# Performance work log

Measured on AMD Instinct MI355X. Metric: run time of the kernel, lower is better.

The kernel has to match this reference:

```python
import jax, jax.numpy as jnp
import numpy as np

BN_EPS = 1e-5
N_SH, N_SS, N_HH, D = 1195, 390, 805, 64


def _gcn(x, edge_index, W, b, n_nodes, mean):
    # per-edge message = Linear(x_j); lin(x)[src] == lin(x[src])
    h = x @ W + b                                   # [N, out]
    msg = h[edge_index[0]]                          # gather sources -> [E, out]
    agg = jax.ops.segment_sum(msg, edge_index[1], num_segments=n_nodes)
    if mean:
        cnt = jax.ops.segment_sum(jnp.ones((edge_index.shape[1],), x.dtype),
                                  edge_index[1], num_segments=n_nodes)
        agg = agg / jnp.maximum(cnt, 1.0)[:, None]
    return jnp.tanh(agg)


def _bn(x, gamma, beta):
    # BatchNorm1d in training mode: biased batch statistics
    m = jnp.mean(x, axis=0)
    v = jnp.var(x, axis=0)
    return (x - m) * jax.lax.rsqrt(v + BN_EPS) * gamma + beta


def setup_inputs() -> dict:
    key = jax.random.key(0)
    ks = jax.random.split(key, 40)
    f32 = jnp.float32

    def lin(k, din, dout):
        k1, k2 = jax.random.split(k)
        s = 1.0 / np.sqrt(din)
        W = jax.random.uniform(k1, (din, dout), f32, -s, s)
        b = jax.random.uniform(k2, (dout,), f32, -s, s)
        return W, b

    inp = {}
    inp["x_SH"] = jnp.arange(N_SH, dtype=jnp.int64 if jax.config.jax_enable_x64 else jnp.int32)
    inp["edge_index_SH"] = jax.random.randint(ks[0], (2, 1_000_000), 0, N_SH)
    inp["x_SS"] = jnp.arange(N_SS)
    inp["edge_index_SS"] = jax.random.randint(ks[1], (2, 200_000), 0, N_SS)
    inp["x_HH"] = jnp.arange(N_HH)
    inp["edge_index_HH"] = jax.random.randint(ks[2], (2, 200_000), 0, N_HH)
    inp["prescription"] = jax.random.uniform(ks[3], (20000, N_SS), f32)
    inp["kgOneHot"] = jax.random.uniform(ks[4], (N_HH, 27), f32)

    inp["emb"] = jax.random.normal(ks[5], (N_SH, D), f32)
    inp["w_sh1"], inp["b_sh1"] = lin(ks[6], D, D)
    inp["w_sh2"], inp["b_sh2"] = lin(ks[7], D, D)
    inp["w_mlp1"], inp["b_mlp1"] = lin(ks[8], D, 256)
    inp["g_bn1"] = jnp.ones((256,), f32); inp["be_bn1"] = jnp.zeros((256,), f32)
    inp["w_sh1h"], inp["b_sh1h"] = lin(ks[9], D, D)
    inp["w_sh2h"], inp["b_sh2h"] = lin(ks[10], D, D)
    inp["w_mlp1h"], inp["b_mlp1h"] = lin(ks[11], D, 256)
    inp["g_bn1h"] = jnp.ones((256,), f32); inp["be_bn1h"] = jnp.zeros((256,), f32)
    inp["w_ss"], inp["b_ss"] = lin(ks[12], D, 256)
    inp["w_hh"], inp["b_hh"] = lin(ks[13], D + 27, 256)
    inp["w_mlp"], inp["b_mlp"] = lin(ks[14], 256, 256)
    inp["g_si"] = jnp.ones((256,), f32); inp["be_si"] = jnp.zeros((256,), f32)
    return inp


def reference(x_SH, edge_index_SH, x_SS, edge_index_SS, x_HH, edge_index_HH,
              prescription, kgOneHot, emb,
              w_sh1, b_sh1, w_sh2, b_sh2, w_mlp1, b_mlp1, g_bn1, be_bn1,
              w_sh1h, b_sh1h, w_sh2h, b_sh2h, w_mlp1h, b_mlp1h, g_bn1h, be_bn1h,
              w_ss, b_ss, w_hh, b_hh, w_mlp, b_mlp, g_si, be_si):
    # symptom branch on SH graph (mean aggregation)
    x1 = emb[x_SH]                                           # [1195, 64]
    x2 = _gcn(x1, edge_index_SH, w_sh1, b_sh1, N_SH, mean=True)
    x6 = _gcn(x2, edge_index_SH, w_sh2, b_sh2, N_SH, mean=True)
    x9 = (x1 + x2 + x6) / 3.0
    x9 = jnp.tanh(_bn(x9 @ w_mlp1 + b_mlp1, g_bn1, be_bn1))  # [1195, 256]

    # herb branch on SH graph
    x22 = _gcn(x1, edge_index_SH, w_sh1h, b_sh1h, N_SH, mean=True)
    x66 = _gcn(x22, edge_index_SH, w_sh2h, b_sh2h, N_SH, mean=True)
    x99 = (x1 + x22 + x66) / 3.0
    x99 = jnp.tanh(_bn(x99 @ w_mlp1h + b_mlp1h, g_bn1h, be_bn1h))

    # SS graph (add aggregation)
    x_ss1 = _gcn(emb[x_SS], edge_index_SS, w_ss, b_ss, N_SS, mean=False)  # [390, 256]

    # HH graph with KG one-hot features appended
    x_hh0 = jnp.concatenate([emb[x_HH], kgOneHot], axis=-1)  # [805, 91]
    x_hh1 = _gcn(x_hh0, edge_index_HH, w_hh, b_hh, N_HH, mean=False)      # [805, 256]

    es = x9[:N_SS] + x_ss1                                   # [390, 256]
    eh = x99[N_SS:] + x_hh1                                  # [805, 256]

    e_synd = prescription @ es                               # [B, 256]
    pre_sum = jnp.sum(prescription, axis=1, keepdims=True)
    e = e_synd / pre_sum
    e = jax.nn.relu(_bn(e @ w_mlp + b_mlp, g_si, be_si))
    return e @ eh.T                                          # [B, 805]
```

## Files before the change

### kernel.cpp

```cpp
#include <hip/hip_runtime.h>
#include <cstddef>
#include <cstdint>

#define N_SH 1195
#define N_SS 390
#define N_HH 805
#define DIM  64

typedef __bf16 bf16_t;
typedef bf16_t bf16x4v __attribute__((ext_vector_type(4)));
typedef bf16_t bf16x8v __attribute__((ext_vector_type(8)));
typedef float f32x4 __attribute__((ext_vector_type(4)));

__device__ inline ushort f2bf(float f) {
    union { float f; uint32_t u; } c; c.f = f;
    uint32_t u = c.u;
    u += 0x7FFFu + ((u >> 16) & 1u);
    return (ushort)(u >> 16);
}

__device__ inline void xcd_swizzle(int gx, int gy, int& bx, int& by) {
    int nwg = gx * gy;
    int lin = by * gx + bx;
    int q = nwg >> 3, r = nwg & 7;
    int xcd = lin & 7, idx = lin >> 3;
    int nt = (xcd < r ? xcd * (q + 1) : r * (q + 1) + (xcd - r) * q) + idx;
    by = nt / gx; bx = nt % gx;
}

__global__ void build_adj3_kernel(
    const int* __restrict__ e1, int E1, int hs1, uint32_t* __restrict__ T1,
    const int* __restrict__ e2, int E2, int hs2, uint32_t* __restrict__ T2,
    const int* __restrict__ e3, int E3, int hs3, uint32_t* __restrict__ T3)
{
    int i = blockIdx.x * blockDim.x + threadIdx.x;
    if (i < E1) {
        int src = e1[i], dst = e1[E1 + i];
        atomicAdd(&T1[(size_t)dst * hs1 + (src >> 2)], 1u << ((src & 3) * 8));
    } else if (i < E1 + E2) {
        int j = i - E1;
        int src = e2[j], dst = e2[E2 + j];
        atomicAdd(&T2[(size_t)dst * hs2 + (src >> 2)], 1u << ((src & 3) * 8));
    } else if (i < E1 + E2 + E3) {
        int j = i - E1 - E2;
        int src = e3[j], dst = e3[E3 + j];
        atomicAdd(&T3[(size_t)dst * hs3 + (src >> 2)], 1u << ((src & 3) * 8));
    }
}

__global__ void rowsum_inv_packed_kernel(const uint32_t* __restrict__ T, int R,
                                         int halfStride, float* __restrict__ inv) {
    int row  = blockIdx.x * (blockDim.x / 64) + (threadIdx.x / 64);
    int lane = threadIdx.x & 63;
    if (row >= R) return;
    const uint32_t* p = T + (size_t)row * halfStride;
    uint32_t s = 0;
    for (int c = lane; c < halfStride; c += 64) {
        uint32_t w = p[c];
        s += (w & 0xFFu) + ((w >> 8) & 0xFFu) + ((w >> 16) & 0xFFu) + (w >> 24);
    }
    for (int off = 32; off > 0; off >>= 1) s += __shfl_down(s, off);
    if (lane == 0) inv[row] = 1.0f / fmaxf((float)s, 1.0f);
}

__device__ inline void unpack_one(const uint32_t* __restrict__ T, int R, int C,
                                  int hs, ushort* __restrict__ out, int Cp, int i) {
    int r = i / Cp, c = i % Cp;
    float v = 0.f;
    if (r < R && c < C) {
        uint32_t w = T[(size_t)r * hs + (c >> 2)];
        v = (float)((w >> ((c & 3) * 8)) & 0xFFu);
    }
    out[i] = f2bf(v);
}

__global__ void cvt_unpack3_kernel(
    const uint32_t* __restrict__ T1, int hs1, ushort* __restrict__ o1, int n1, int Cp1,
    const uint32_t* __restrict__ T2, int hs2, ushort* __restrict__ o2, int n2, int Cp2,
    const uint32_t* __restrict__ T3, int hs3, ushort* __restrict__ o3, int n3, int Cp3)
{
    int i = blockIdx.x * blockDim.x + threadIdx.x;
    if (i < n1) { unpack_one(T1, N_SH, N_SH, hs1, o1, Cp1, i); return; }
    i -= n1;
    if (i < n2) { unpack_one(T2, N_SS, N_SS, hs2, o2, Cp2, i); return; }
    i -= n2;
    if (i < n3) { unpack_one(T3, N_HH, N_HH, hs3, o3, Cp3, i); }
}

#define BM 64
#define BN 64
#define BK 16

__global__ __launch_bounds__(256) void gemm_kernel(
    const float* __restrict__ A, const float* __restrict__ A2, int ldaA, int ldaA2,
    const float* __restrict__ B,
    const float* __restrict__ bias,
    float* __restrict__ C, ushort* __restrict__ outT, int ldt,
    int M, int N, int K, float* __restrict__ statsOut, int statsStride)
{
    __shared__ float As[BK][BM + 4];
    __shared__ float Bs[BK][BN];
    __shared__ float cs[128];
    const int tid  = threadIdx.x;
    const int row0 = blockIdx.y * BM;
    const int col0 = blockIdx.x * BN;
    const int tr  = (tid >> 4) << 2;
    const int tc  = (tid & 15) << 2;
    const int lar = tid >> 2;
    const int lac = (tid & 3) << 2;
    const int lbr = tid >> 4;
    const int lbc = (tid & 15) << 2;

    float acc[4][4] = {{0.f}};

    for (int k0 = 0; k0 < K; k0 += BK) {
        const int gr = row0 + lar;
        #pragma unroll
        for (int i = 0; i < 4; ++i) {
            int gk = k0 + lac + i;
            float v = 0.f;
            if (gr < M && gk < K) {
                v = A[(size_t)gr * ldaA + gk];
                if (A2) v += A2[(size_t)gr * ldaA2 + gk];
            }
            As[lac + i][lar] = v;
        }
        const int gk = k0 + lbr;
        const float* Bp = B + (size_t)gk * N + col0 + lbc;
        #pragma unroll
        for (int i = 0; i < 4; ++i) {
            int gc = col0 + lbc + i;
            Bs[lbr][lbc + i] = (gk < K && gc < N) ? Bp[i] : 0.f;
        }
        __syncthreads();
        #pragma unroll
        for (int kk = 0; kk < BK; ++kk) {
            float4 a = *reinterpret_cast<const float4*>(&As[kk][tr]);
            float4 b = *reinterpret_cast<const float4*>(&Bs[kk][tc]);
            acc[0][0] += a.x * b.x; acc[0][1] += a.x * b.y; acc[0][2] += a.x * b.z; acc[0][3] += a.x * b.w;
            acc[1][0] += a.y * b.x; acc[1][1] += a.y * b.y; acc[1][2] += a.y * b.z; acc[1][3] += a.y * b.w;
            acc[2][0] += a.z * b.x; acc[2][1] += a.z * b.y; acc[2][2] += a.z * b.z; acc[2][3] += a.z * b.w;
            acc[3][0] += a.w * b.x; acc[3][1] += a.w * b.y; acc[3][2] += a.w * b.z; acc[3][3] += a.w * b.w;
        }
        __syncthreads();
    }

    float ls[4] = {0.f, 0.f, 0.f, 0.f}, lq[4] = {0.f, 0.f, 0.f, 0.f};
    #pragma unroll
    for (int i = 0; i < 4; ++i) {
        int gr = row0 + tr + i;
        if (gr >= M) continue;
        #pragma unroll
        for (int j = 0; j < 4; ++j) {
            int gc = col0 + tc + j;
            if (gc >= N) continue;
            float v = acc[i][j];
            if (bias) v += bias[gc];
            if (outT) outT[(size_t)gc * ldt + gr] = f2bf(v);
            else      C[(size_t)gr * N + gc] = v;
            ls[j] += v; lq[j] += v * v;
        }
    }

    if (statsOut) {
        if (tid < 128) cs[tid] = 0.f;
        __syncthreads();
        #pragma unroll
        for (int j = 0; j < 4; ++j) {
            atomicAdd(&cs[tc + j], ls[j]);
            atomicAdd(&cs[64 + tc + j], lq[j]);
        }
        __syncthreads();
        if (tid < 64) {
            atomicAdd(&statsOut[col0 + tid], cs[tid]);
            atomicAdd(&statsOut[statsStride + col0 + tid], cs[64 + tid]);
// ... 133 lines not shown
    }

    __syncthreads();
    #pragma unroll
    for (int n = 0; n < 4; ++n) {
        int lc = wc * 64 + n * 16 + l15;
        atomicAdd(&cs[lc], ls[n]);
        atomicAdd(&cs[128 + lc], lq[n]);
    }
    __syncthreads();
    if (tid < 128) {
        atomicAdd(&statsOut[col0 + tid], cs[tid]);
        atomicAdd(&statsOut[256 + col0 + tid], cs[128 + tid]);
    }
}

__global__ __launch_bounds__(256) void mfma_c3_kernel(
    const float* __restrict__ Abuf, const ushort* __restrict__ Bt,
    int M, int Nw,
    const float* __restrict__ stats, const float* __restrict__ g,
    const float* __restrict__ be,
    float* __restrict__ outF, int ldo)
{
    __shared__ __align__(16) ushort As[128 * LDT];
    __shared__ __align__(16) ushort Bs[128 * LDT];
    __shared__ float sscale[256], sshift[256];
    const int tid  = threadIdx.x;
    int bx = blockIdx.x, by = blockIdx.y;
    xcd_swizzle(gridDim.x, gridDim.y, bx, by);
    const int row0 = by * 128;
    const int col0 = bx * 128;
    const int wid  = tid >> 6, lane = tid & 63;
    const int wr = wid >> 1, wc = wid & 1;
    const int l15 = lane & 15, lg = lane >> 4;
    const int kg = lg * 4;
    const int sr = tid >> 2;
    const int sc = (tid & 3) * 8;

    if (tid < 256) {
        float invM = 1.0f / (float)M;
        float mean = stats[tid] * invM;
        float var  = fmaxf(stats[256 + tid] * invM - mean * mean, 0.f);
        float scv  = g[tid] * rsqrtf(var + 1e-5f);
        sscale[tid] = scv;
        sshift[tid] = be[tid] - mean * scv;
    }
    __syncthreads();

    const float*  pA0 = Abuf + (size_t)(row0 + sr)      * 256 + sc;
    const float*  pA1 = Abuf + (size_t)(row0 + sr + 64) * 256 + sc;
    const ushort* pB0 = Bt + (size_t)(col0 + sr)        * 256 + sc;
    const ushort* pB1 = Bt + (size_t)(col0 + sr + 64)   * 256 + sc;

    float4 a00 = *reinterpret_cast<const float4*>(pA0);
    float4 a01 = *reinterpret_cast<const float4*>(pA0 + 4);
    float4 a10 = *reinterpret_cast<const float4*>(pA1);
    float4 a11 = *reinterpret_cast<const float4*>(pA1 + 4);
    uint4  b0  = *reinterpret_cast<const uint4*>(pB0);
    uint4  b1  = *reinterpret_cast<const uint4*>(pB1);

    f32x4 acc[4][4];
    #pragma unroll
    for (int m = 0; m < 4; ++m)
        #pragma unroll
        for (int n = 0; n < 4; ++n) acc[m][n] = (f32x4)0.f;

    for (int k0 = 0; k0 < 256; k0 += 32) {
        float s8[8], t8[8];
        #pragma unroll
        for (int i = 0; i < 8; ++i) { s8[i] = sscale[k0 + sc + i]; t8[i] = sshift[k0 + sc + i]; }
        {
            bf16_t h[8];
            h[0] = (bf16_t)fmaxf(a00.x * s8[0] + t8[0], 0.f);
            h[1] = (bf16_t)fmaxf(a00.y * s8[1] + t8[1], 0.f);
            h[2] = (bf16_t)fmaxf(a00.z * s8[2] + t8[2], 0.f);
            h[3] = (bf16_t)fmaxf(a00.w * s8[3] + t8[3], 0.f);
            h[4] = (bf16_t)fmaxf(a01.x * s8[4] + t8[4], 0.f);
            h[5] = (bf16_t)fmaxf(a01.y * s8[5] + t8[5], 0.f);
            h[6] = (bf16_t)fmaxf(a01.z * s8[6] + t8[6], 0.f);
            h[7] = (bf16_t)fmaxf(a01.w * s8[7] + t8[7], 0.f);
            *reinterpret_cast<uint4*>(&As[sr * LDT + sc]) = *reinterpret_cast<const uint4*>(h);
            h[0] = (bf16_t)fmaxf(a10.x * s8[0] + t8[0], 0.f);
            h[1] = (bf16_t)fmaxf(a10.y * s8[1] + t8[1], 0.f);
            h[2] = (bf16_t)fmaxf(a10.z * s8[2] + t8[2], 0.f);
            h[3] = (bf16_t)fmaxf(a10.w * s8[3] + t8[3], 0.f);
            h[4] = (bf16_t)fmaxf(a11.x * s8[4] + t8[4], 0.f);
            h[5] = (bf16_t)fmaxf(a11.y * s8[5] + t8[5], 0.f);
            h[6] = (bf16_t)fmaxf(a11.z * s8[6] + t8[6], 0.f);
            h[7] = (bf16_t)fmaxf(a11.w * s8[7] + t8[7], 0.f);
            *reinterpret_cast<uint4*>(&As[(sr + 64) * LDT + sc]) = *reinterpret_cast<const uint4*>(h);
        }
        *reinterpret_cast<uint4*>(&Bs[sr * LDT + sc])        = b0;
        *reinterpret_cast<uint4*>(&Bs[(sr + 64) * LDT + sc]) = b1;
        __syncthreads();
        if (k0 + 32 < 256) {
            a00 = *reinterpret_cast<const float4*>(pA0 + k0 + 32);
            a01 = *reinterpret_cast<const float4*>(pA0 + k0 + 36);
            a10 = *reinterpret_cast<const float4*>(pA1 + k0 + 32);
            a11 = *reinterpret_cast<const float4*>(pA1 + k0 + 36);
            b0  = *reinterpret_cast<const uint4*>(pB0 + k0 + 32);
            b1  = *reinterpret_cast<const uint4*>(pB1 + k0 + 32);
        }

        bf16x8v af[4], bfr[4];
        #pragma unroll
        for (int m = 0; m < 4; ++m) {
            int ar = wr * 64 + m * 16 + l15;
            bf16x4v lo = *reinterpret_cast<const bf16x4v*>(&As[ar * LDT + kg]);
            bf16x4v hi = *reinterpret_cast<const bf16x4v*>(&As[ar * LDT + kg + 16]);
            af[m] = __builtin_shufflevector(lo, hi, 0, 1, 2, 3, 4, 5, 6, 7);
        }
        #pragma unroll
        for (int n = 0; n < 4; ++n) {
            int br = wc * 64 + n * 16 + l15;
            bf16x4v lo = *reinterpret_cast<const bf16x4v*>(&Bs[br * LDT + kg]);
            bf16x4v hi = *reinterpret_cast<const bf16x4v*>(&Bs[br * LDT + kg + 16]);
            bfr[n] = __builtin_shufflevector(lo, hi, 0, 1, 2, 3, 4, 5, 6, 7);
        }
        #pragma unroll
        for (int m = 0; m < 4; ++m)
            #pragma unroll
            for (int n = 0; n < 4; ++n)
                acc[m][n] = __builtin_amdgcn_mfma_f32_16x16x32_bf16(af[m], bfr[n], acc[m][n], 0, 0, 0);
        __syncthreads();
    }

    #pragma unroll
    for (int m = 0; m < 4; ++m) {
        int grow_base = row0 + wr * 64 + m * 16 + kg;
        #pragma unroll
        for (int j = 0; j < 4; ++j) {
            int grow = grow_base + j;
            if (grow >= M) continue;
            #pragma unroll
            for (int n = 0; n < 4; ++n) {
                int gcol = col0 + wc * 64 + n * 16 + l15;
                if (gcol >= Nw) continue;
                outF[(size_t)grow * ldo + gcol] = acc[m][n][j];
            }
        }
    }
}

__global__ __launch_bounds__(256) void mfma_splitk_kernel(
    const ushort* __restrict__ A, const ushort* __restrict__ Bt,
    int M, int K, int lda, int kChunk, int Ntot,
    float* __restrict__ part)
{
    __shared__ __align__(16) ushort As[128 * LDT];
    __shared__ __align__(16) ushort Bs[128 * LDT];
    const int tid  = threadIdx.x;
    const int row0 = blockIdx.y * 128;
    const int col0 = blockIdx.x * 128;
    const int wid  = tid >> 6, lane = tid & 63;
    const int wr = wid >> 1, wc = wid & 1;
    const int l15 = lane & 15, lg = lane >> 4;
    const int kg = lg * 4;
    const int sr = tid >> 2;
    const int sc = (tid & 3) * 8;

    const int k0s = blockIdx.z * kChunk;
    const int k0e = (k0s + kChunk < K) ? k0s + kChunk : K;

    const ushort* pA0 = A  + (size_t)(row0 + sr)      * lda + sc;
    const ushort* pA1 = A  + (size_t)(row0 + sr + 64) * lda + sc;
    const ushort* pB0 = Bt + (size_t)(col0 + sr)      * lda + sc;
    const ushort* pB1 = Bt + (size_t)(col0 + sr + 64) * lda + sc;

    uint4 ra0 = *reinterpret_cast<const uint4*>(pA0 + k0s);
    uint4 ra1 = *reinterpret_cast<const uint4*>(pA1 + k0s);
    uint4 rb0 = *reinterpret_cast<const uint4*>(pB0 + k0s);
    uint4 rb1 = *reinterpret_cast<const uint4*>(pB1 + k0s);

    f32x4 acc[4][4];
    #pragma unroll
    for (int m = 0; m < 4; ++m)
        #pragma unroll
        for (int n = 0; n < 4; ++n) acc[m][n] = (f32x4)0.f;
// ... 17 lines not shown
            int ar = wr * 64 + m * 16 + l15;
            bf16x4v lo = *reinterpret_cast<const bf16x4v*>(&As[ar * LDT + kg]);
            bf16x4v hi = *reinterpret_cast<const bf16x4v*>(&As[ar * LDT + kg + 16]);
            af[m] = __builtin_shufflevector(lo, hi, 0, 1, 2, 3, 4, 5, 6, 7);
        }
        #pragma unroll
        for (int n = 0; n < 4; ++n) {
            int br = wc * 64 + n * 16 + l15;
            bf16x4v lo = *reinterpret_cast<const bf16x4v*>(&Bs[br * LDT + kg]);
            bf16x4v hi = *reinterpret_cast<const bf16x4v*>(&Bs[br * LDT + kg + 16]);
            bfr[n] = __builtin_shufflevector(lo, hi, 0, 1, 2, 3, 4, 5, 6, 7);
        }
        #pragma unroll
        for (int m = 0; m < 4; ++m)
            #pragma unroll
            for (int n = 0; n < 4; ++n)
                acc[m][n] = __builtin_amdgcn_mfma_f32_16x16x32_bf16(af[m], bfr[n], acc[m][n], 0, 0, 0);
        __syncthreads();
    }

    float* pslab = part + (size_t)blockIdx.z * M * Ntot;
    #pragma unroll
    for (int m = 0; m < 4; ++m) {
        int grow_base = row0 + wr * 64 + m * 16 + kg;
        #pragma unroll
        for (int j = 0; j < 4; ++j) {
            int grow = grow_base + j;
            if (grow >= M) continue;
            #pragma unroll
            for (int n = 0; n < 4; ++n) {
                int gcol = col0 + wc * 64 + n * 16 + l15;
                pslab[(size_t)grow * Ntot + gcol] = acc[m][n][j];
            }
        }
    }
}

__global__ void reduce_tanh_kernel(const float* __restrict__ part, int S, int M, int N,
                                   const float* __restrict__ rs,
                                   const float* __restrict__ emb,
                                   const float* __restrict__ prev,
                                   float* __restrict__ out) {
    int i = blockIdx.x * blockDim.x + threadIdx.x;
    if (i >= M * N) return;
    int r = i / N, j = i - r * N;
    float s = 0.f;
    for (int z = 0; z < S; ++z) s += part[(size_t)z * M * N + i];
    if (rs) s *= rs[r];
    float t = tanhf(s);
    if (emb) out[i] = (emb[r * 64 + (j & 63)] + prev[i] + t) * (1.0f / 3.0f);
    else     out[i] = t;
}

__global__ void make_cat_weights_kernel(
    const float* __restrict__ w_sh1, const float* __restrict__ w_sh1h,
    const float* __restrict__ b_sh1, const float* __restrict__ b_sh1h,
    const float* __restrict__ w_sh2, const float* __restrict__ w_sh2h,
    const float* __restrict__ b_sh2, const float* __restrict__ b_sh2h,
    const float* __restrict__ w_mlp1, const float* __restrict__ w_mlp1h,
    const float* __restrict__ b_mlp1, const float* __restrict__ b_mlp1h,
    float* __restrict__ W1cat, float* __restrict__ b1cat,
    float* __restrict__ W2bd,  float* __restrict__ b2cat,
    float* __restrict__ WMbd,  float* __restrict__ bMcat)
{
    int i = blockIdx.x * blockDim.x + threadIdx.x;
    if (i < 64 * 128) {
        int k = i >> 7, j = i & 127;
        W1cat[i] = (j < 64) ? w_sh1[k * 64 + j] : w_sh1h[k * 64 + (j - 64)];
        return;
    }
    i -= 64 * 128;
    if (i < 128) { b1cat[i] = (i < 64) ? b_sh1[i] : b_sh1h[i - 64]; return; }
    i -= 128;
    if (i < 128 * 128) {
        int k = i >> 7, j = i & 127;
        float v = 0.f;
        if (k < 64 && j < 64) v = w_sh2[k * 64 + j];
        else if (k >= 64 && j >= 64) v = w_sh2h[(k - 64) * 64 + (j - 64)];
        W2bd[i] = v;
        return;
    }
    i -= 128 * 128;
    if (i < 128) { b2cat[i] = (i < 64) ? b_sh2[i] : b_sh2h[i - 64]; return; }
    i -= 128;
    if (i < 128 * 512) {
        int k = i >> 9, j = i & 511;
        float v = 0.f;
        if (j < 256) { if (k < 64) v = w_mlp1[k * 256 + j]; }
        else         { if (k >= 64) v = w_mlp1h[(k - 64) * 256 + (j - 256)]; }
        WMbd[i] = v;
        return;
    }
    i -= 128 * 512;
    if (i < 512) { bMcat[i] = (i < 256) ? b_mlp1[i] : b_mlp1h[i - 256]; }
}

__global__ void concat_hh_kernel(const float* __restrict__ emb, const float* __restrict__ kg,
                                 float* __restrict__ out) {
    int i = blockIdx.x * blockDim.x + threadIdx.x;
    const int n = N_HH * 91;
    if (i >= n) return;
    int r = i / 91, c = i % 91;
    out[i] = (c < DIM) ? emb[r * DIM + c] : kg[r * 27 + (c - DIM)];
}

__global__ void make_ehb_kernel(const float* __restrict__ x9cat, const float* __restrict__ hh1,
                                ushort* __restrict__ out, int Rp) {
    int i = blockIdx.x * blockDim.x + threadIdx.x;
    if (i >= Rp * 256) return;
    int r = i >> 8, c = i & 255;
    float v = (r < N_HH) ? (x9cat[(size_t)(N_SS + r) * 512 + 256 + c] + hh1[(size_t)r * 256 + c]) : 0.f;
    out[i] = f2bf(v);
}

__global__ void bn_apply_cat_kernel(const float* __restrict__ X, const float* __restrict__ stats,
                                    const float* __restrict__ g1, const float* __restrict__ be1,
                                    const float* __restrict__ g2, const float* __restrict__ be2,
                                    int M, float* __restrict__ out) {
    int i = blockIdx.x * blockDim.x + threadIdx.x;
    if (i >= M * 512) return;
    int j = i & 511;
    float invM = 1.0f / (float)M;
    float mean = stats[j] * invM;
    float var  = fmaxf(stats[512 + j] * invM - mean * mean, 0.f);
    float ga = (j < 256) ? g1[j]  : g2[j - 256];
    float bb = (j < 256) ? be1[j] : be2[j - 256];
    float y = (X[i] - mean) * rsqrtf(var + 1e-5f) * ga + bb;
    out[i] = tanhf(y);
}

extern "C" void kernel_launch(void* const* d_in, const int* in_sizes, int n_in,
                              void* d_out, int out_size, void* d_ws, size_t ws_size,
                              hipStream_t stream) {
    const int*   eiSH = (const int*)d_in[1];
    const int*   eiSS = (const int*)d_in[3];
    const int*   eiHH = (const int*)d_in[5];
    const float* P    = (const float*)d_in[6];
    const float* kg   = (const float*)d_in[7];
    const float* emb  = (const float*)d_in[8];
    const float* w_sh1  = (const float*)d_in[9];   const float* b_sh1  = (const float*)d_in[10];
    const float* w_sh2  = (const float*)d_in[11];  const float* b_sh2  = (const float*)d_in[12];
    const float* w_mlp1 = (const float*)d_in[13];  const float* b_mlp1 = (const float*)d_in[14];
    const float* g_bn1  = (const float*)d_in[15];  const float* be_bn1 = (const float*)d_in[16];
    const float* w_sh1h = (const float*)d_in[17];  const float* b_sh1h = (const float*)d_in[18];
    const float* w_sh2h = (const float*)d_in[19];  const float* b_sh2h = (const float*)d_in[20];
    const float* w_mlp1h= (const float*)d_in[21];  const float* b_mlp1h= (const float*)d_in[22];
    const float* g_bn1h = (const float*)d_in[23];  const float* be_bn1h= (const float*)d_in[24];
    const float* w_ss   = (const float*)d_in[25];  const float* b_ss   = (const float*)d_in[26];
    const float* w_hh   = (const float*)d_in[27];  const float* b_hh   = (const float*)d_in[28];
    const float* w_mlp  = (const float*)d_in[29];  const float* b_mlp  = (const float*)d_in[30];
    const float* g_si   = (const float*)d_in[31];  const float* be_si  = (const float*)d_in[32];
    float* out = (float*)d_out;

    const int E_SH = in_sizes[1] / 2;
    const int E_SS = in_sizes[3] / 2;
    const int E_HH = in_sizes[5] / 2;
    const int B    = in_sizes[6] / N_SS;
    const int Mp   = ((B + 127) / 128) * 128;
    const int KP1  = 416;
    const int NP3  = 896;
    const int KSH  = 1216;
    const int KHH  = 832;
    const int HS_SH = (N_SH + 3) / 4;
    const int HS_SS = (N_SS + 3) / 4;
    const int HS_HH = (N_HH + 3) / 4;

    float* w = (float*)d_ws;
    size_t off = 0;
    auto alloc = [&](size_t n) { float* p = w + off; off += (n + 3) & ~(size_t)3; return p; };

    float* cntInv   = alloc(N_SH);
    float* statsCat = alloc(1024);
    float* statsC2  = alloc(512);
    ushort* HT      = (ushort*)alloc((size_t)128 * KSH / 2);
    ushort* HSST    = (ushort*)alloc((size_t)256 * KP1 / 2);
    ushort* HHHT    = (ushort*)alloc((size_t)256 * KHH / 2);
    ushort* eswT    = (ushort*)alloc((size_t)256 * KP1 / 2);
    float* zeroEnd  = w + off;
    float* W1cat   = alloc(64 * 128);
    float* b1cat   = alloc(128);
    float* W2bd    = alloc(128 * 128);
    float* b2cat   = alloc(128);
    float* WMbd    = alloc(128 * 512);
    float* bMcat   = alloc(512);
    ushort* adjb   = (ushort*)alloc((size_t)1280 * KSH / 2);
    ushort* adjSSb = (ushort*)alloc((size_t)512 * KP1 / 2);
    ushort* adjHHb = (ushort*)alloc((size_t)896 * KHH / 2);
    float* x2cat   = alloc((size_t)N_SH * 128);
    float* x9a2    = alloc((size_t)N_SH * 128);
    float* tmpBN   = alloc((size_t)N_SH * 512);
    float* x9cat   = alloc((size_t)N_SH * 512);
    float* ss1     = alloc((size_t)N_SS * 256);
    float* hh1     = alloc((size_t)N_HH * 256);
    float* xhh0    = alloc((size_t)N_HH * 91);
    ushort* eh_b   = (ushort*)alloc((size_t)NP3 * 256 / 2);
    float* regionA = alloc((size_t)Mp * 256);
    uint32_t* uSH  = (uint32_t*)regionA;
    uint32_t* uSS  = uSH + (size_t)N_SH * HS_SH;
    uint32_t* uHH  = uSS + (size_t)N_SS * HS_SS;
    size_t packed_words = (size_t)N_SH * HS_SH + (size_t)N_SS * HS_SS + (size_t)N_HH * HS_HH;
    float*  bufM   = regionA;
    float* regionB = alloc((size_t)Mp * 256);
    float*  partials = regionB;
    (void)ws_size; (void)n_in; (void)out_size;

    auto gemmT = [&](const float* Am, const float* A2m, int lda1, int lda2,
                     const float* Bm, const float* bias,
                     ushort* oT, int ldt, int M, int N, int K) {
        dim3 g((N + BN - 1) / BN, (M + BM - 1) / BM);
        gemm_kernel<<<g, 256, 0, stream>>>(Am, A2m, lda1, lda2, Bm, bias,
                                           nullptr, oT, ldt, M, N, K, nullptr, 0);
    };
    auto gemmF = [&](const float* Am, const float* Bm, const float* bias,
                     float* C, int M, int N, int K, float* st, int sstride) {
        dim3 g((N + BN - 1) / BN, (M + BM - 1) / BM);
        gemm_kernel<<<g, 256, 0, stream>>>(Am, nullptr, K, 0, Bm, bias,
                                           C, nullptr, 0, M, N, K, st, sstride);
    };
    auto splitk = [&](const ushort* Am, const ushort* Bm, int M, int Mtiles, int K, int lda,
                      int Ntot, int S, const float* rs, const float* embA, const float* prev,
                      float* outp) {
        dim3 g(Ntot / 128, Mtiles, S);
        mfma_splitk_kernel<<<g, 256, 0, stream>>>(Am, Bm, M, K, lda, 128, Ntot, partials);
        reduce_tanh_kernel<<<(M * Ntot + 255) / 256, 256, 0, stream>>>(
            partials, S, M, Ntot, rs, embA, prev, outp);
    };

    hipMemsetAsync(uSH, 0, packed_words * sizeof(uint32_t), stream);
    hipMemsetAsync(statsCat, 0, (size_t)((char*)zeroEnd - (char*)statsCat), stream);

    {
        int Etot = E_SH + E_SS + E_HH;
        build_adj3_kernel<<<(Etot + 255) / 256, 256, 0, stream>>>(
            eiSH, E_SH, HS_SH, uSH, eiSS, E_SS, HS_SS, uSS, eiHH, E_HH, HS_HH, uHH);
    }
    rowsum_inv_packed_kernel<<<(N_SH + 3) / 4, 256, 0, stream>>>(uSH, N_SH, HS_SH, cntInv);
    {
        int n1 = 1280 * KSH, n2 = 512 * KP1, n3 = 896 * KHH;
        cvt_unpack3_kernel<<<(n1 + n2 + n3 + 255) / 256, 256, 0, stream>>>(
            uSH, HS_SH, adjb, n1, KSH, uSS, HS_SS, adjSSb, n2, KP1, uHH, HS_HH, adjHHb, n3, KHH);
    }

    make_cat_weights_kernel<<<(90880 + 255) / 256, 256, 0, stream>>>(
        w_sh1, w_sh1h, b_sh1, b_sh1h, w_sh2, w_sh2h, b_sh2, b_sh2h,
        w_mlp1, w_mlp1h, b_mlp1, b_mlp1h,
        W1cat, b1cat, W2bd, b2cat, WMbd, bMcat);

    gemmT(emb, nullptr, 64, 0, W1cat, b1cat, HT, KSH, N_SH, 128, 64);
    splitk(adjb, HT, N_SH, 10, KSH, KSH, 128, 10, cntInv, nullptr, nullptr, x2cat);
    gemmT(x2cat, nullptr, 128, 0, W2bd, b2cat, HT, KSH, N_SH, 128, 128);
    splitk(adjb, HT, N_SH, 10, KSH, KSH, 128, 10, cntInv, emb, x2cat, x9a2);
    gemmF(x9a2, WMbd, bMcat, tmpBN, N_SH, 512, 128, statsCat, 512);
    bn_apply_cat_kernel<<<(N_SH * 512 + 255) / 256, 256, 0, stream>>>(
        tmpBN, statsCat, g_bn1, be_bn1, g_bn1h, be_bn1h, N_SH, x9cat);

    gemmT(emb, nullptr, 64, 0, w_ss, b_ss, HSST, KP1, N_SS, 256, 64);
    splitk(adjSSb, HSST, N_SS, 4, KP1, KP1, 256, 4, nullptr, nullptr, nullptr, ss1);

    concat_hh_kernel<<<(N_HH * 91 + 255) / 256, 256, 0, stream>>>(emb, kg, xhh0);
    gemmT(xhh0, nullptr, 91, 0, w_hh, b_hh, HHHT, KHH, N_HH, 256, 91);
    splitk(adjHHb, HHHT, N_HH, 7, KHH, KHH, 256, 7, nullptr, nullptr, nullptr, hh1);

    make_ehb_kernel<<<(NP3 * 256 + 255) / 256, 256, 0, stream>>>(x9cat, hh1, eh_b, NP3);

    gemmT(x9cat, ss1, 512, 256, w_mlp, nullptr, eswT, KP1, N_SS, 256, 256);
    {
        dim3 g(2, (B + 127) / 128);
        mfma_c1_kernel<<<g, 256, 0, stream>>>(P, eswT, B, b_mlp, bufM, statsC2);
    }
    {
        dim3 g(NP3 / 128, (B + 127) / 128);
        mfma_c3_kernel<<<g, 256, 0, stream>>>(bufM, eh_b, B, N_HH, statsC2, g_si, be_si, out, N_HH);
    }
}
```

Baseline: 315.3 us.

## Merge prep kernels, fuse BN+tanh into consumers, double-buffer c3 loop, finer split-K

Folds the row-sum, weight concatenation and HH concat kernels into the adjacency unpack kernel, so one launch does all preprocessing. The standalone BN-apply pass is removed: BN+tanh is now applied on the fly in the es GEMM's A-load and in the eh bf16 builder, which drops the x9cat buffer and its write/read traffic. The c3 MFMA loop now holds two register prefetch stages covering 64 K-values per iteration, and split-K uses 64-wide K chunks, so there are more splits. The costs are branchy, divergent mega-kernel code, tanh recomputed per GEMM tile load, and more split-K partials to reduce.

```diff
diff --git a/kernel.cpp b/kernel.cpp
--- a/kernel.cpp
+++ b/kernel.cpp
@@ -48,21 +48,6 @@
     }
 }
 
-__global__ void rowsum_inv_packed_kernel(const uint32_t* __restrict__ T, int R,
-                                         int halfStride, float* __restrict__ inv) {
-    int row  = blockIdx.x * (blockDim.x / 64) + (threadIdx.x / 64);
-    int lane = threadIdx.x & 63;
-    if (row >= R) return;
-    const uint32_t* p = T + (size_t)row * halfStride;
-    uint32_t s = 0;
-    for (int c = lane; c < halfStride; c += 64) {
-        uint32_t w = p[c];
-        s += (w & 0xFFu) + ((w >> 8) & 0xFFu) + ((w >> 16) & 0xFFu) + (w >> 24);
-    }
-    for (int off = 32; off > 0; off >>= 1) s += __shfl_down(s, off);
-    if (lane == 0) inv[row] = 1.0f / fmaxf((float)s, 1.0f);
-}
-
 __device__ inline void unpack_one(const uint32_t* __restrict__ T, int R, int C,
                                   int hs, ushort* __restrict__ out, int Cp, int i) {
     int r = i / Cp, c = i % Cp;
@@ -74,17 +59,77 @@
     out[i] = f2bf(v);
 }
 
-__global__ void cvt_unpack3_kernel(
+__global__ void mega_prep_kernel(
     const uint32_t* __restrict__ T1, int hs1, ushort* __restrict__ o1, int n1, int Cp1,
     const uint32_t* __restrict__ T2, int hs2, ushort* __restrict__ o2, int n2, int Cp2,
-    const uint32_t* __restrict__ T3, int hs3, ushort* __restrict__ o3, int n3, int Cp3)
+    const uint32_t* __restrict__ T3, int hs3, ushort* __restrict__ o3, int n3, int Cp3,
+    float* __restrict__ cntInv,
+    const float* __restrict__ w_sh1, const float* __restrict__ w_sh1h,
+    const float* __restrict__ b_sh1, const float* __restrict__ b_sh1h,
+    const float* __restrict__ w_sh2, const float* __restrict__ w_sh2h,
+    const float* __restrict__ b_sh2, const float* __restrict__ b_sh2h,
+    const float* __restrict__ w_mlp1, const float* __restrict__ w_mlp1h,
+    const float* __restrict__ b_mlp1, const float* __restrict__ b_mlp1h,
+    float* __restrict__ W1cat, float* __restrict__ b1cat,
+    float* __restrict__ W2bd,  float* __restrict__ b2cat,
+    float* __restrict__ WMbd,  float* __restrict__ bMcat,
+    const float* __restrict__ emb, const float* __restrict__ kg,
+    float* __restrict__ xhh0)
 {
     int i = blockIdx.x * blockDim.x + threadIdx.x;
     if (i < n1) { unpack_one(T1, N_SH, N_SH, hs1, o1, Cp1, i); return; }
     i -= n1;
     if (i < n2) { unpack_one(T2, N_SS, N_SS, hs2, o2, Cp2, i); return; }
     i -= n2;
-    if (i < n3) { unpack_one(T3, N_HH, N_HH, hs3, o3, Cp3, i); }
+    if (i < n3) { unpack_one(T3, N_HH, N_HH, hs3, o3, Cp3, i); return; }
+    i -= n3;
+    if (i < N_SH * 64) {
+        int row = i >> 6, lane = i & 63;
+        const uint32_t* p = T1 + (size_t)row * hs1;
+        uint32_t s = 0;
+        for (int c = lane; c < hs1; c += 64) {
+            uint32_t w0 = p[c];
+            s += (w0 & 0xFFu) + ((w0 >> 8) & 0xFFu) + ((w0 >> 16) & 0xFFu) + (w0 >> 24);
+        }
+        for (int off = 32; off > 0; off >>= 1) s += __shfl_down(s, off);
+        if (lane == 0) cntInv[row] = 1.0f / fmaxf((float)s, 1.0f);
+        return;
+    }
+    i -= N_SH * 64;
+    if (i < 64 * 128) {
+        int k = i >> 7, j = i & 127;
+        W1cat[i] = (j < 64) ? w_sh1[k * 64 + j] : w_sh1h[k * 64 + (j - 64)];
+        return;
+    }
+    i -= 64 * 128;
+    if (i < 128) { b1cat[i] = (i < 64) ? b_sh1[i] : b_sh1h[i - 64]; return; }
+    i -= 128;
+    if (i < 128 * 128) {
+        int k = i >> 7, j = i & 127;
+        float v = 0.f;
+        if (k < 64 && j < 64) v = w_sh2[k * 64 + j];
+        else if (k >= 64 && j >= 64) v = w_sh2h[(k - 64) * 64 + (j - 64)];
+        W2bd[i] = v;
+        return;
+    }
+    i -= 128 * 128;
+    if (i < 128) { b2cat[i] = (i < 64) ? b_sh2[i] : b_sh2h[i - 64]; return; }
+    i -= 128;
+    if (i < 128 * 512) {
+        int k = i >> 9, j = i & 511;
+        float v = 0.f;
+        if (j < 256) { if (k < 64) v = w_mlp1[k * 256 + j]; }
+        else         { if (k >= 64) v = w_mlp1h[(k - 64) * 256 + (j - 256)]; }
+        WMbd[i] = v;
+        return;
+    }
+    i -= 128 * 512;
+    if (i < 512) { bMcat[i] = (i < 256) ? b_mlp1[i] : b_mlp1h[i - 256]; return; }
+    i -= 512;
+    if (i < N_HH * 91) {
+        int r = i / 91, c = i % 91;
+        xhh0[i] = (c < DIM) ? emb[r * DIM + c] : kg[r * 27 + (c - DIM)];
+    }
 }
 
 #define BM 64
@@ -96,11 +141,14 @@
     const float* __restrict__ B,
     const float* __restrict__ bias,
     float* __restrict__ C, ushort* __restrict__ outT, int ldt,
-    int M, int N, int K, float* __restrict__ statsOut, int statsStride)
+    int M, int N, int K, float* __restrict__ statsOut, int statsStride,
+    const float* __restrict__ bnStats, const float* __restrict__ bnG,
+    const float* __restrict__ bnBe, int bnM)
 {
     __shared__ float As[BK][BM + 4];
     __shared__ float Bs[BK][BN];
     __shared__ float cs[128];
+    __shared__ float sA[256], tA[256];
     const int tid  = threadIdx.x;
     const int row0 = blockIdx.y * BM;
     const int col0 = blockIdx.x * BN;
@@ -111,6 +159,16 @@
     const int lbr = tid >> 4;
     const int lbc = (tid & 15) << 2;
 
+    if (bnStats) {
+        float invM = 1.0f / (float)bnM;
+        float mean = bnStats[tid] * invM;
+        float var  = fmaxf(bnStats[512 + tid] * invM - mean * mean, 0.f);
+        float scv  = bnG[tid] * rsqrtf(var + 1e-5f);
+        sA[tid] = scv;
+        tA[tid] = bnBe[tid] - mean * scv;
+        __syncthreads();
+    }
+
     float acc[4][4] = {{0.f}};
 
     for (int k0 = 0; k0 < K; k0 += BK) {
@@ -121,6 +179,7 @@
             float v = 0.f;
             if (gr < M && gk < K) {
                 v = A[(size_t)gr * ldaA + gk];
+                if (bnStats) v = tanhf(v * sA[gk] + tA[gk]);
                 if (A2) v += A2[(size_t)gr * ldaA2 + gk];
             }
             As[lac + i][lar] = v;
@@ -360,12 +419,18 @@
     const ushort* pB0 = Bt + (size_t)(col0 + sr)        * 256 + sc;
     const ushort* pB1 = Bt + (size_t)(col0 + sr + 64)   * 256 + sc;
 
-    float4 a00 = *reinterpret_cast<const float4*>(pA0);
-    float4 a01 = *reinterpret_cast<const float4*>(pA0 + 4);
-    float4 a10 = *reinterpret_cast<const float4*>(pA1);
-    float4 a11 = *reinterpret_cast<const float4*>(pA1 + 4);
-    uint4  b0  = *reinterpret_cast<const uint4*>(pB0);
-    uint4  b1  = *reinterpret_cast<const uint4*>(pB1);
+    float4 xa00 = *reinterpret_cast<const float4*>(pA0);
+    float4 xa01 = *reinterpret_cast<const float4*>(pA0 + 4);
+    float4 xa10 = *reinterpret_cast<const float4*>(pA1);
+    float4 xa11 = *reinterpret_cast<const float4*>(pA1 + 4);
+    uint4  xb0  = *reinterpret_cast<const uint4*>(pB0);
+    uint4  xb1  = *reinterpret_cast<const uint4*>(pB1);
+    float4 ya00 = *reinterpret_cast<const float4*>(pA0 + 32);
+    float4 ya01 = *reinterpret_cast<const float4*>(pA0 + 36);
+    float4 ya10 = *reinterpret_cast<const float4*>(pA1 + 32);
+    float4 ya11 = *reinterpret_cast<const float4*>(pA1 + 36);
+    uint4  yb0  = *reinterpret_cast<const uint4*>(pB0 + 32);
+    uint4  yb1  = *reinterpret_cast<const uint4*>(pB1 + 32);
 
     f32x4 acc[4][4];
     #pragma unroll
@@ -373,65 +438,90 @@
         #pragma unroll
         for (int n = 0; n < 4; ++n) acc[m][n] = (f32x4)0.f;
 
-    for (int k0 = 0; k0 < 256; k0 += 32) {
-        float s8[8], t8[8];
-        #pragma unroll
-        for (int i = 0; i < 8; ++i) { s8[i] = sscale[k0 + sc + i]; t8[i] = sshift[k0 + sc + i]; }
-        {
-            bf16_t h[8];
-            h[0] = (bf16_t)fmaxf(a00.x * s8[0] + t8[0], 0.f);
-            h[1] = (bf16_t)fmaxf(a00.y * s8[1] + t8[1], 0.f);
-            h[2] = (bf16_t)fmaxf(a00.z * s8[2] + t8[2], 0.f);
-            h[3] = (bf16_t)fmaxf(a00.w * s8[3] + t8[3], 0.f);
-            h[4] = (bf16_t)fmaxf(a01.x * s8[4] + t8[4], 0.f);
-            h[5] = (bf16_t)fmaxf(a01.y * s8[5] + t8[5], 0.f);
-            h[6] = (bf16_t)fmaxf(a01.z * s8[6] + t8[6], 0.f);
-            h[7] = (bf16_t)fmaxf(a01.w * s8[7] + t8[7], 0.f);
-            *reinterpret_cast<uint4*>(&As[sr * LDT + sc]) = *reinterpret_cast<const uint4*>(h);
-            h[0] = (bf16_t)fmaxf(a10.x * s8[0] + t8[0], 0.f);
-            h[1] = (bf16_t)fmaxf(a10.y * s8[1] + t8[1], 0.f);
-            h[2] = (bf16_t)fmaxf(a10.z * s8[2] + t8[2], 0.f);
-            h[3] = (bf16_t)fmaxf(a10.w * s8[3] + t8[3], 0.f);
-            h[4] = (bf16_t)fmaxf(a11.x * s8[4] + t8[4], 0.f);
-            h[5] = (bf16_t)fmaxf(a11.y * s8[5] + t8[5], 0.f);
-            h[6] = (bf16_t)fmaxf(a11.z * s8[6] + t8[6], 0.f);
-            h[7] = (bf16_t)fmaxf(a11.w * s8[7] + t8[7], 0.f);
-            *reinterpret_cast<uint4*>(&As[(sr + 64) * LDT + sc]) = *reinterpret_cast<const uint4*>(h);
-        }
-        *reinterpret_cast<uint4*>(&Bs[sr * LDT + sc])        = b0;
-        *reinterpret_cast<uint4*>(&Bs[(sr + 64) * LDT + sc]) = b1;
-        __syncthreads();
-        if (k0 + 32 < 256) {
-            a00 = *reinterpret_cast<const float4*>(pA0 + k0 + 32);
-            a01 = *reinterpret_cast<const float4*>(pA0 + k0 + 36);
-            a10 = *reinterpret_cast<const float4*>(pA1 + k0 + 32);
-            a11 = *reinterpret_cast<const float4*>(pA1 + k0 + 36);
-            b0  = *reinterpret_cast<const uint4*>(pB0 + k0 + 32);
-            b1  = *reinterpret_cast<const uint4*>(pB1 + k0 + 32);
-        }
-
-        bf16x8v af[4], bfr[4];
-        #pragma unroll
-        for (int m = 0; m < 4; ++m) {
-            int ar = wr * 64 + m * 16 + l15;
-            bf16x4v lo = *reinterpret_cast<const bf16x4v*>(&As[ar * LDT + kg]);
-            bf16x4v hi = *reinterpret_cast<const bf16x4v*>(&As[ar * LDT + kg + 16]);
-            af[m] = __builtin_shufflevector(lo, hi, 0, 1, 2, 3, 4, 5, 6, 7);
-        }
-        #pragma unroll
-        for (int n = 0; n < 4; ++n) {
-            int br = wc * 64 + n * 16 + l15;
-            bf16x4v lo = *reinterpret_cast<const bf16x4v*>(&Bs[br * LDT + kg]);
-            bf16x4v hi = *reinterpret_cast<const bf16x4v*>(&Bs[br * LDT + kg + 16]);
-            bfr[n] = __builtin_shufflevector(lo, hi, 0, 1, 2, 3, 4, 5, 6, 7);
-        }
-        #pragma unroll
-        for (int m = 0; m < 4; ++m)
-            #pragma unroll
-            for (int n = 0; n < 4; ++n)
-                acc[m][n] = __builtin_amdgcn_mfma_f32_16x16x32_bf16(af[m], bfr[n], acc[m][n], 0, 0, 0);
-        __syncthreads();
-    }
+    #define C3_STAGE(A00,A01,A10,A11,B0,B1,KOFF)                                     \
+        {                                                                            \
+            float s8[8], t8[8];                                                      \
+            _Pragma("unroll")                                                        \
+            for (int i = 0; i < 8; ++i) { s8[i] = sscale[(KOFF) + sc + i];           \
+                                          t8[i] = sshift[(KOFF) + sc + i]; }         \
+            bf16_t h[8];                                                             \
+            h[0] = (bf16_t)fmaxf(A00.x * s8[0] + t8[0], 0.f);                        \
+            h[1] = (bf16_t)fmaxf(A00.y * s8[1] + t8[1], 0.f);                        \
+            h[2] = (bf16_t)fmaxf(A00.z * s8[2] + t8[2], 0.f);                        \
+            h[3] = (bf16_t)fmaxf(A00.w * s8[3] + t8[3], 0.f);                        \
+            h[4] = (bf16_t)fmaxf(A01.x * s8[4] + t8[4], 0.f);                        \
+            h[5] = (bf16_t)fmaxf(A01.y * s8[5] + t8[5], 0.f);                        \
+            h[6] = (bf16_t)fmaxf(A01.z * s8[6] + t8[6], 0.f);                        \
+            h[7] = (bf16_t)fmaxf(A01.w * s8[7] + t8[7], 0.f);                        \
+            *reinterpret_cast<uint4*>(&As[sr * LDT + sc]) =                          \
+                *reinterpret_cast<const uint4*>(h);                                  \
+            h[0] = (bf16_t)fmaxf(A10.x * s8[0] + t8[0], 0.f);                        \
+            h[1] = (bf16_t)fmaxf(A10.y * s8[1] + t8[1], 0.f);                        \
+            h[2] = (bf16_t)fmaxf(A10.z * s8[2] + t8[2], 0.f);                        \
+            h[3] = (bf16_t)fmaxf(A10.w * s8[3] + t8[3], 0.f);                        \
+            h[4] = (bf16_t)fmaxf(A11.x * s8[4] + t8[4], 0.f);                        \
+            h[5] = (bf16_t)fmaxf(A11.y * s8[5] + t8[5], 0.f);                        \
+            h[6] = (bf16_t)fmaxf(A11.z * s8[6] + t8[6], 0.f);                        \
+            h[7] = (bf16_t)fmaxf(A11.w * s8[7] + t8[7], 0.f);                        \
+            *reinterpret_cast<uint4*>(&As[(sr + 64) * LDT + sc]) =                   \
+                *reinterpret_cast<const uint4*>(h);                                  \
+            *reinterpret_cast<uint4*>(&Bs[sr * LDT + sc])        = B0;               \
+            *reinterpret_cast<uint4*>(&Bs[(sr + 64) * LDT + sc]) = B1;               \
+        }
+
+    #define C3_COMPUTE()                                                             \
+        {                                                                            \
+            bf16x8v af[4], bfr[4];                                                   \
+            _Pragma("unroll")                                                        \
+            for (int m = 0; m < 4; ++m) {                                            \
+                int ar = wr * 64 + m * 16 + l15;                                     \
+                bf16x4v lo = *reinterpret_cast<const bf16x4v*>(&As[ar * LDT + kg]);  \
+                bf16x4v hi = *reinterpret_cast<const bf16x4v*>(&As[ar * LDT + kg + 16]); \
+                af[m] = __builtin_shufflevector(lo, hi, 0, 1, 2, 3, 4, 5, 6, 7);     \
+            }                                                                        \
+            _Pragma("unroll")                                                        \
+            for (int n = 0; n < 4; ++n) {                                            \
+                int br = wc * 64 + n * 16 + l15;                                     \
+                bf16x4v lo = *reinterpret_cast<const bf16x4v*>(&Bs[br * LDT + kg]);  \
+                bf16x4v hi = *reinterpret_cast<const bf16x4v*>(&Bs[br * LDT + kg + 16]); \
+                bfr[n] = __builtin_shufflevector(lo, hi, 0, 1, 2, 3, 4, 5, 6, 7);    \
+            }                                                                        \
+            _Pragma("unroll")                                                        \
+            for (int m = 0; m < 4; ++m)                                              \
+                _Pragma("unroll")                                                    \
+                for (int n = 0; n < 4; ++n)                                          \
+                    acc[m][n] = __builtin_amdgcn_mfma_f32_16x16x32_bf16(             \
+                        af[m], bfr[n], acc[m][n], 0, 0, 0);                          \
+        }
+
+    for (int k0 = 0; k0 < 256; k0 += 64) {
+        C3_STAGE(xa00, xa01, xa10, xa11, xb0, xb1, k0);
+        __syncthreads();
+        if (k0 + 64 < 256) {
+            xa00 = *reinterpret_cast<const float4*>(pA0 + k0 + 64);
+            xa01 = *reinterpret_cast<const float4*>(pA0 + k0 + 68);
+            xa10 = *reinterpret_cast<const float4*>(pA1 + k0 + 64);
+            xa11 = *reinterpret_cast<const float4*>(pA1 + k0 + 68);
+            xb0  = *reinterpret_cast<const uint4*>(pB0 + k0 + 64);
+            xb1  = *reinterpret_cast<const uint4*>(pB1 + k0 + 64);
+        }
+        C3_COMPUTE();
+        __syncthreads();
+        C3_STAGE(ya00, ya01, ya10, ya11, yb0, yb1, k0 + 32);
+        __syncthreads();
+        if (k0 + 96 < 256) {
+            ya00 = *reinterpret_cast<const float4*>(pA0 + k0 + 96);
+            ya01 = *reinterpret_cast<const float4*>(pA0 + k0 + 100);
+            ya10 = *reinterpret_cast<const float4*>(pA1 + k0 + 96);
+            ya11 = *reinterpret_cast<const float4*>(pA1 + k0 + 100);
+            yb0  = *reinterpret_cast<const uint4*>(pB0 + k0 + 96);
+            yb1  = *reinterpret_cast<const uint4*>(pB1 + k0 + 96);
+        }
+        C3_COMPUTE();
+        __syncthreads();
+    }
+    #undef C3_STAGE
+    #undef C3_COMPUTE
 
     #pragma unroll
     for (int m = 0; m < 4; ++m) {
@@ -555,81 +645,25 @@
     else     out[i] = t;
 }
 
-__global__ void make_cat_weights_kernel(
-    const float* __restrict__ w_sh1, const float* __restrict__ w_sh1h,
-    const float* __restrict__ b_sh1, const float* __restrict__ b_sh1h,
-    const float* __restrict__ w_sh2, const float* __restrict__ w_sh2h,
-    const float* __restrict__ b_sh2, const float* __restrict__ b_sh2h,
-    const float* __restrict__ w_mlp1, const float* __restrict__ w_mlp1h,
-    const float* __restrict__ b_mlp1, const float* __restrict__ b_mlp1h,
-    float* __restrict__ W1cat, float* __restrict__ b1cat,
-    float* __restrict__ W2bd,  float* __restrict__ b2cat,
-    float* __restrict__ WMbd,  float* __restrict__ bMcat)
-{
-    int i = blockIdx.x * blockDim.x + threadIdx.x;
-    if (i < 64 * 128) {
-        int k = i >> 7, j = i & 127;
-        W1cat[i] = (j < 64) ? w_sh1[k * 64 + j] : w_sh1h[k * 64 + (j - 64)];
-        return;
-    }
-    i -= 64 * 128;
-    if (i < 128) { b1cat[i] = (i < 64) ? b_sh1[i] : b_sh1h[i - 64]; return; }
-    i -= 128;
-    if (i < 128 * 128) {
-        int k = i >> 7, j = i & 127;
-        float v = 0.f;
-        if (k < 64 && j < 64) v = w_sh2[k * 64 + j];
-        else if (k >= 64 && j >= 64) v = w_sh2h[(k - 64) * 64 + (j - 64)];
-        W2bd[i] = v;
-        return;
-    }
-    i -= 128 * 128;
-    if (i < 128) { b2cat[i] = (i < 64) ? b_sh2[i] : b_sh2h[i - 64]; return; }
-    i -= 128;
-    if (i < 128 * 512) {
-        int k = i >> 9, j = i & 511;
-        float v = 0.f;
-        if (j < 256) { if (k < 64) v = w_mlp1[k * 256 + j]; }
-        else         { if (k >= 64) v = w_mlp1h[(k - 64) * 256 + (j - 256)]; }
-        WMbd[i] = v;
-        return;
-    }
-    i -= 128 * 512;
-    if (i < 512) { bMcat[i] = (i < 256) ? b_mlp1[i] : b_mlp1h[i - 256]; }
-}
-
-__global__ void concat_hh_kernel(const float* __restrict__ emb, const float* __restrict__ kg,
-                                 float* __restrict__ out) {
-    int i = blockIdx.x * blockDim.x + threadIdx.x;
-    const int n = N_HH * 91;
-    if (i >= n) return;
-    int r = i / 91, c = i % 91;
-    out[i] = (c < DIM) ? emb[r * DIM + c] : kg[r * 27 + (c - DIM)];
-}
-
-__global__ void make_ehb_kernel(const float* __restrict__ x9cat, const float* __restrict__ hh1,
-                                ushort* __restrict__ out, int Rp) {
+__global__ void make_ehb_bn_kernel(const float* __restrict__ tmpBN,
+                                   const float* __restrict__ stats,
+                                   const float* __restrict__ g, const float* __restrict__ be,
+                                   const float* __restrict__ hh1,
+                                   ushort* __restrict__ out, int Rp) {
     int i = blockIdx.x * blockDim.x + threadIdx.x;
     if (i >= Rp * 256) return;
     int r = i >> 8, c = i & 255;
-    float v = (r < N_HH) ? (x9cat[(size_t)(N_SS + r) * 512 + 256 + c] + hh1[(size_t)r * 256 + c]) : 0.f;
+    float v = 0.f;
+    if (r < N_HH) {
+        float invM = 1.0f / (float)N_SH;
+        int j = 256 + c;
+        float mean = stats[j] * invM;
+        float var  = fmaxf(stats[512 + j] * invM - mean * mean, 0.f);
+        float x = tmpBN[(size_t)(N_SS + r) * 512 + j];
+        float y = tanhf((x - mean) * rsqrtf(var + 1e-5f) * g[c] + be[c]);
+        v = y + hh1[(size_t)r * 256 + c];
+    }
     out[i] = f2bf(v);
-}
-
-__global__ void bn_apply_cat_kernel(const float* __restrict__ X, const float* __restrict__ stats,
-                                    const float* __restrict__ g1, const float* __restrict__ be1,
-                                    const float* __restrict__ g2, const float* __restrict__ be2,
-                                    int M, float* __restrict__ out) {
-    int i = blockIdx.x * blockDim.x + threadIdx.x;
-    if (i >= M * 512) return;
-    int j = i & 511;
-    float invM = 1.0f / (float)M;
-    float mean = stats[j] * invM;
-    float var  = fmaxf(stats[512 + j] * invM - mean * mean, 0.f);
-    float ga = (j < 256) ? g1[j]  : g2[j - 256];
-    float bb = (j < 256) ? be1[j] : be2[j - 256];
-    float y = (X[i] - mean) * rsqrtf(var + 1e-5f) * ga + bb;
-    out[i] = tanhf(y);
 }
 
 extern "C" void kernel_launch(void* const* d_in, const int* in_sizes, int n_in,
@@ -692,7 +726,6 @@
     float* x2cat   = alloc((size_t)N_SH * 128);
     float* x9a2    = alloc((size_t)N_SH * 128);
     float* tmpBN   = alloc((size_t)N_SH * 512);
-    float* x9cat   = alloc((size_t)N_SH * 512);
     float* ss1     = alloc((size_t)N_SS * 256);
     float* hh1     = alloc((size_t)N_HH * 256);
     float* xhh0    = alloc((size_t)N_HH * 91);
@@ -709,22 +742,26 @@
 
     auto gemmT = [&](const float* Am, const float* A2m, int lda1, int lda2,
                      const float* Bm, const float* bias,
-                     ushort* oT, int ldt, int M, int N, int K) {
+                     ushort* oT, int ldt, int M, int N, int K,
+                     const float* bnS, const float* bnG, const float* bnB, int bnM) {
         dim3 g((N + BN - 1) / BN, (M + BM - 1) / BM);
         gemm_kernel<<<g, 256, 0, stream>>>(Am, A2m, lda1, lda2, Bm, bias,
-                                           nullptr, oT, ldt, M, N, K, nullptr, 0);
+                                           nullptr, oT, ldt, M, N, K, nullptr, 0,
+                                           bnS, bnG, bnB, bnM);
     };
     auto gemmF = [&](const float* Am, const float* Bm, const float* bias,
                      float* C, int M, int N, int K, float* st, int sstride) {
         dim3 g((N + BN - 1) / BN, (M + BM - 1) / BM);
         gemm_kernel<<<g, 256, 0, stream>>>(Am, nullptr, K, 0, Bm, bias,
-                                           C, nullptr, 0, M, N, K, st, sstride);
+                                           C, nullptr, 0, M, N, K, st, sstride,
+                                           nullptr, nullptr, nullptr, 0);
     };
     auto splitk = [&](const ushort* Am, const ushort* Bm, int M, int Mtiles, int K, int lda,
-                      int Ntot, int S, const float* rs, const float* embA, const float* prev,
+                      int Ntot, const float* rs, const float* embA, const float* prev,
                       float* outp) {
+        int S = (K + 63) / 64;
         dim3 g(Ntot / 128, Mtiles, S);
-        mfma_splitk_kernel<<<g, 256, 0, stream>>>(Am, Bm, M, K, lda, 128, Ntot, partials);
+        mfma_splitk_kernel<<<g, 256, 0, stream>>>(Am, Bm, M, K, lda, 64, Ntot, partials);
         reduce_tanh_kernel<<<(M * Ntot + 255) / 256, 256, 0, stream>>>(
             partials, S, M, Ntot, rs, embA, prev, outp);
     };
@@ -737,36 +774,39 @@
         build_adj3_kernel<<<(Etot + 255) / 256, 256, 0, stream>>>(
             eiSH, E_SH, HS_SH, uSH, eiSS, E_SS, HS_SS, uSS, eiHH, E_HH, HS_HH, uHH);
     }
-    rowsum_inv_packed_kernel<<<(N_SH + 3) / 4, 256, 0, stream>>>(uSH, N_SH, HS_SH, cntInv);
     {
         int n1 = 1280 * KSH, n2 = 512 * KP1, n3 = 896 * KHH;
-        cvt_unpack3_kernel<<<(n1 + n2 + n3 + 255) / 256, 256, 0, stream>>>(
-            uSH, HS_SH, adjb, n1, KSH, uSS, HS_SS, adjSSb, n2, KP1, uHH, HS_HH, adjHHb, n3, KHH);
-    }
-
-    make_cat_weights_kernel<<<(90880 + 255) / 256, 256, 0, stream>>>(
-        w_sh1, w_sh1h, b_sh1, b_sh1h, w_sh2, w_sh2h, b_sh2, b_sh2h,
-        w_mlp1, w_mlp1h, b_mlp1, b_mlp1h,
-        W1cat, b1cat, W2bd, b2cat, WMbd, bMcat);
-
-    gemmT(emb, nullptr, 64, 0, W1cat, b1cat, HT, KSH, N_SH, 128, 64);
-    splitk(adjb, HT, N_SH, 10, KSH, KSH, 128, 10, cntInv, nullptr, nullptr, x2cat);
-    gemmT(x2cat, nullptr, 128, 0, W2bd, b2cat, HT, KSH, N_SH, 128, 128);
-    splitk(adjb, HT, N_SH, 10, KSH, KSH, 128, 10, cntInv, emb, x2cat, x9a2);
+        int tot = n1 + n2 + n3 + N_SH * 64 + 90880 + N_HH * 91;
+        mega_prep_kernel<<<(tot + 255) / 256, 256, 0, stream>>>(
+            uSH, HS_SH, adjb, n1, KSH, uSS, HS_SS, adjSSb, n2, KP1,
+            uHH, HS_HH, adjHHb, n3, KHH, cntInv,
+            w_sh1, w_sh1h, b_sh1, b_sh1h, w_sh2, w_sh2h, b_sh2, b_sh2h,
+            w_mlp1, w_mlp1h, b_mlp1, b_mlp1h,
+            W1cat, b1cat, W2bd, b2cat, WMbd, bMcat,
+            emb, kg, xhh0);
+    }
+
+    gemmT(emb, nullptr, 64, 0, W1cat, b1cat, HT, KSH, N_SH, 128, 64,
+          nullptr, nullptr, nullptr, 0);
+    splitk(adjb, HT, N_SH, 10, KSH, KSH, 128, cntInv, nullptr, nullptr, x2cat);
+    gemmT(x2cat, nullptr, 128, 0, W2bd, b2cat, HT, KSH, N_SH, 128, 128,
+          nullptr, nullptr, nullptr, 0);
+    splitk(adjb, HT, N_SH, 10, KSH, KSH, 128, cntInv, emb, x2cat, x9a2);
     gemmF(x9a2, WMbd, bMcat, tmpBN, N_SH, 512, 128, statsCat, 512);
-    bn_apply_cat_kernel<<<(N_SH * 512 + 255) / 256, 256, 0, stream>>>(
-        tmpBN, statsCat, g_bn1, be_bn1, g_bn1h, be_bn1h, N_SH, x9cat);
-
-    gemmT(emb, nullptr, 64, 0, w_ss, b_ss, HSST, KP1, N_SS, 256, 64);
-    splitk(adjSSb, HSST, N_SS, 4, KP1, KP1, 256, 4, nullptr, nullptr, nullptr, ss1);
-
-    concat_hh_kernel<<<(N_HH * 91 + 255) / 256, 256, 0, stream>>>(emb, kg, xhh0);
-    gemmT(xhh0, nullptr, 91, 0, w_hh, b_hh, HHHT, KHH, N_HH, 256, 91);
-    splitk(adjHHb, HHHT, N_HH, 7, KHH, KHH, 256, 7, nullptr, nullptr, nullptr, hh1);
-
-    make_ehb_kernel<<<(NP3 * 256 + 255) / 256, 256, 0, stream>>>(x9cat, hh1, eh_b, NP3);
-
-    gemmT(x9cat, ss1, 512, 256, w_mlp, nullptr, eswT, KP1, N_SS, 256, 256);
+
+    gemmT(emb, nullptr, 64, 0, w_ss, b_ss, HSST, KP1, N_SS, 256, 64,
+          nullptr, nullptr, nullptr, 0);
+    splitk(adjSSb, HSST, N_SS, 4, KP1, KP1, 256, nullptr, nullptr, nullptr, ss1);
+
+    gemmT(xhh0, nullptr, 91, 0, w_hh, b_hh, HHHT, KHH, N_HH, 256, 91,
+          nullptr, nullptr, nullptr, 0);
+    splitk(adjHHb, HHHT, N_HH, 7, KHH, KHH, 256, nullptr, nullptr, nullptr, hh1);
+
+    make_ehb_bn_kernel<<<(NP3 * 256 + 255) / 256, 256, 0, stream>>>(
+        tmpBN, statsCat, g_bn1h, be_bn1h, hh1, eh_b, NP3);
+
+    gemmT(tmpBN, ss1, 512, 256, w_mlp, nullptr, eswT, KP1, N_SS, 256, 256,
+          statsCat, g_bn1, be_bn1, N_SH);
     {
         dim3 g(2, (B + 127) / 128);
         mfma_c1_kernel<<<g, 256, 0, stream>>>(P, eswT, B, b_mlp, bufM, statsC2);
```

Measured after the change: 329.5 us. +4.5%, slower.
